# Performance work log

Measured on AMD Instinct MI355X. Metric: run time of the kernel, lower is better.

The kernel has to match this reference:

```python
import jax, jax.numpy as jnp
import numpy as np

N_NODES = 100000
N_EDGES = 3200000
IN_CH, HID, OUT_CH = 11, 64, 1


def setup_inputs() -> dict:
    key = jax.random.key(0)
    ks = jax.random.split(key, 10)
    x = jax.random.normal(ks[0], (N_NODES, IN_CH), dtype=jnp.float32)
    edge_index = jax.random.randint(ks[1], (2, N_EDGES), 0, N_NODES, dtype=jnp.int64)
    s = lambda k, shape, fan_in: jax.random.normal(k, shape, jnp.float32) * (1.0 / np.sqrt(fan_in))
    return {
        "x": x,
        "edge_index": edge_index,
        # conv1: lin_l acts on aggregated neighbors (has bias), lin_r on root (no bias)
        "Wl1": s(ks[2], (HID, IN_CH), IN_CH), "bl1": jnp.zeros((HID,), jnp.float32),
        "Wr1": s(ks[3], (HID, IN_CH), IN_CH),
        "Wl2": s(ks[4], (HID, HID), HID), "bl2": jnp.zeros((HID,), jnp.float32),
        "Wr2": s(ks[5], (HID, HID), HID),
        "Wlin": s(ks[6], (OUT_CH, HID), HID), "blin": jnp.zeros((OUT_CH,), jnp.float32),
    }


def _sage_conv(x, src, dst, Wl, bl, Wr):
    # mean aggregation of source features onto destination nodes
    msg = x[src]                                            # [E, d] gather
    agg = jax.ops.segment_sum(msg, dst, num_segments=N_NODES)          # [N, d]
    cnt = jax.ops.segment_sum(jnp.ones_like(dst, jnp.float32), dst, num_segments=N_NODES)
    mean = agg / jnp.maximum(cnt, 1.0)[:, None]             # isolated nodes -> 0
    return mean @ Wl.T + bl + x @ Wr.T


def reference(x, edge_index, Wl1, bl1, Wr1, Wl2, bl2, Wr2, Wlin, blin):
    src, dst = edge_index[0], edge_index[1]
    h = jax.nn.relu(_sage_conv(x, src, dst, Wl1, bl1, Wr1))
    h = jax.nn.relu(_sage_conv(h, src, dst, Wl2, bl2, Wr2))
    return h @ Wlin.T + blin
```

## Files before the change

### kernel.cpp

```cpp
#include <hip/hip_runtime.h>
#include <hip/hip_fp16.h>

#define IN_CH 11
#define HID 64
#define PAD 64
#define OVCAP 16384
#define NBLK 512
#define BSH 10

typedef _Float16 half8_t __attribute__((ext_vector_type(8)));
typedef float f32x4_t __attribute__((ext_vector_type(4)));

__global__ void k_prep(const float* __restrict__ x, const float* __restrict__ Wl2,
                       const float* __restrict__ Wr2, unsigned* __restrict__ xphu,
                       __half* __restrict__ wl2h, __half* __restrict__ wr2h,
                       int* __restrict__ ovcnt, int N) {
    int i = blockIdx.x * blockDim.x + threadIdx.x;
    if (i == 0) *ovcnt = 0;
    if (i < HID * HID) {
        wl2h[i] = __float2half_rn(Wl2[i]);
        wr2h[i] = __float2half_rn(Wr2[i]);
    }
    if (i < (N + 1) * 8) {
        int n = i >> 3, j = (i & 7) * 2;
        float a = 0.f, b = 0.f;
        if (n < N) {
            if (j < IN_CH) a = x[n * IN_CH + j];
            if (j + 1 < IN_CH) b = x[n * IN_CH + j + 1];
        }
        unsigned lo = (unsigned)__half_as_ushort(__float2half_rn(a));
        unsigned hi = (unsigned)__half_as_ushort(__float2half_rn(b));
        xphu[i] = lo | (hi << 16);
    }
}


__global__ __launch_bounds__(256) void k_hist(const int* __restrict__ dst,
        int* __restrict__ hist, int E, int csz, int nbkt) {
    __shared__ int h[128];
    int tid = threadIdx.x, blk = blockIdx.x;
    if (tid < 128) h[tid] = 0;
    __syncthreads();
    int c0 = blk * csz, c1 = min(c0 + csz, E);
    for (int e = c0 + tid; e < c1; e += 256)
        atomicAdd(&h[dst[e] >> BSH], 1);
    __syncthreads();
    if (tid < nbkt) hist[tid * NBLK + blk] = h[tid];
}

__global__ __launch_bounds__(512) void k_scanA(int* __restrict__ hist,
        int* __restrict__ btot) {
    __shared__ int wsum[8];
    int b = blockIdx.x, tid = threadIdx.x;
    int lane = tid & 63, wv = tid >> 6;
    int v = hist[b * NBLK + tid];
    int inc = v;
    #pragma unroll
    for (int off = 1; off < 64; off <<= 1) {
        int t = __shfl_up(inc, off);
        if (lane >= off) inc += t;
    }
    if (lane == 63) wsum[wv] = inc;
    __syncthreads();
    int base = 0;
    #pragma unroll
    for (int w = 0; w < 8; w++) base += (w < wv) ? wsum[w] : 0;
    hist[b * NBLK + tid] = base + inc - v;
    if (tid == NBLK - 1) btot[b] = base + inc;
}

__global__ __launch_bounds__(128) void k_scanB(const int* __restrict__ btot,
        int* __restrict__ bstart, int nbkt) {
    __shared__ int wsum[2];
    int tid = threadIdx.x;
    int lane = tid & 63, wv = tid >> 6;
    int v = (tid < nbkt) ? btot[tid] : 0;
    int inc = v;
    #pragma unroll
    for (int off = 1; off < 64; off <<= 1) {
        int t = __shfl_up(inc, off);
        if (lane >= off) inc += t;
    }
    if (lane == 63) wsum[wv] = inc;
    __syncthreads();
    int base = (wv == 1) ? wsum[0] : 0;
    if (tid < nbkt) bstart[tid] = base + inc - v;
}

__global__ __launch_bounds__(256) void k_scatter(const int* __restrict__ src,
        const int* __restrict__ dst, const int* __restrict__ hist,
        const int* __restrict__ bstart,
        unsigned* __restrict__ ebuf, int E, int csz, int nbkt) {
    __shared__ int cur[128];
    int tid = threadIdx.x, blk = blockIdx.x;
    if (tid < nbkt) cur[tid] = hist[tid * NBLK + blk] + bstart[tid];
    __syncthreads();
    int c0 = blk * csz, c1 = min(c0 + csz, E);
    for (int e = c0 + tid; e < c1; e += 256) {
        int d = dst[e], s = src[e];
        int slot = atomicAdd(&cur[d >> BSH], 1);
        ebuf[slot] = ((unsigned)(d & 1023) << 17) | (unsigned)s;
    }
}

__global__ __launch_bounds__(1024) void k_bbuild(const unsigned* __restrict__ ebuf,
        const int* __restrict__ bstart, const int* __restrict__ btot,
        int* __restrict__ cnt, int* __restrict__ col64,
        int* __restrict__ ovcnt, int* __restrict__ ov, int N) {
    __shared__ int lc[1024];
    int tid = threadIdx.x, b = blockIdx.x;
    int lo = b << BSH;
    lc[tid] = 0;
    __syncthreads();
    int cs = bstart[b], cc = btot[b];
    for (int i = tid; i < cc; i += 1024) {
        unsigned v = ebuf[cs + i];
        int dl = (int)(v >> 17), s = (int)(v & 0x1FFFFu);
        int r = atomicAdd(&lc[dl], 1);
        if (r < PAD) {
            col64[(size_t)(lo + dl) * PAD + r] = s;
        } else {
            int q = atomicAdd(ovcnt, 1);
            if (q < OVCAP) { ov[2 * q] = lo + dl; ov[2 * q + 1] = s; }
        }
    }
    __syncthreads();
    int n = lo + tid;
    if (n < N) {
        int d = lc[tid];
        cnt[n] = d;
        if (d > PAD) d = PAD;
        int* row = col64 + (size_t)n * PAD;
        for (int r = d; r < PAD; r++) row[r] = N;
    }
}

__global__ void k_agg1(const unsigned* __restrict__ xphu,
                       const int* __restrict__ col64,
                       float* __restrict__ agg1, int N) {
    int lane = threadIdx.x & 63;
    int n = blockIdx.x * 4 + (threadIdx.x >> 6);
    if (n >= N) return;
    int c8 = lane & 7, sub = lane >> 3;
    const int* cb = col64 + n * PAD;
    int s[8];
    #pragma unroll
    for (int jj = 0; jj < 8; jj++) s[jj] = cb[sub + 8 * jj];
    unsigned v[8];
    #pragma unroll
    for (int jj = 0; jj < 8; jj++) v[jj] = xphu[s[jj] * 8 + c8];
    __half2 a2 = __floats2half2_rn(0.f, 0.f);
    #pragma unroll
    for (int jj = 0; jj < 8; jj++) a2 = __hadd2(a2, *(__half2*)&v[jj]);
    float2 f = __half22float2(a2);
    #pragma unroll
    for (int off = 8; off <= 32; off <<= 1) {
        f.x += __shfl_xor(f.x, off);
        f.y += __shfl_xor(f.y, off);
    }
    if (lane < 8) ((float2*)agg1)[n * 8 + lane] = f;
}

__global__ void k_ov1(const int* __restrict__ ovcnt, const int* __restrict__ ov,
                      const float* __restrict__ x, float* __restrict__ agg1) {
    int c = *ovcnt; if (c > OVCAP) c = OVCAP;
    for (int i = blockIdx.x * blockDim.x + threadIdx.x; i < c;
         i += gridDim.x * blockDim.x) {
        int d = ov[2 * i], s = ov[2 * i + 1];
        for (int ch = 0; ch < IN_CH; ch++)
            atomicAdd(&agg1[d * 16 + ch], x[s * IN_CH + ch]);
    }
}

__global__ void k_dense1(const float* __restrict__ x, const float* __restrict__ agg1,
                         const int* __restrict__ cnt, const float* __restrict__ Wl,
                         const float* __restrict__ bl, const float* __restrict__ Wr,
                         unsigned* __restrict__ h1h, int N) {
    int lane = threadIdx.x & 63;
    int n = blockIdx.x * 4 + (threadIdx.x >> 6);
    if (n > N) return;
    if (n == N) {
        if (lane < 32) h1h[n * 32 + lane] = 0u;
        return;
    }
    int deg = cnt[n];
    float inv = deg > 0 ? 1.f / (float)deg : 0.f;
    float mv = (lane < 16) ? agg1[n * 16 + lane] * inv : 0.f;
    float xv = (lane < IN_CH) ? x[n * IN_CH + lane] : 0.f;
    float h = bl[lane];
    #pragma unroll
    for (int c = 0; c < IN_CH; c++)
        h += Wl[lane * IN_CH + c] * __shfl(mv, c) + Wr[lane * IN_CH + c] * __shfl(xv, c);
    h = fmaxf(h, 0.f);
    unsigned my = (unsigned)__half_as_ushort(__float2half_rn(h));
    unsigned nx = __shfl_down(my, 1);
    if ((lane & 1) == 0) h1h[n * 32 + (lane >> 1)] = my | (nx << 16);
}

__global__ void k_agg2(const uint4* __restrict__ h1h4, const int* __restrict__ col64,
                       float* __restrict__ agg2, int N) {
    int lane = threadIdx.x & 63;
    int n = blockIdx.x * 4 + (threadIdx.x >> 6);
    if (n >= N) return;
    int c8 = lane & 7, sub = lane >> 3;
    const int* cb = col64 + n * PAD;
    int s[8];
    #pragma unroll
    for (int jj = 0; jj < 8; jj++) s[jj] = cb[sub + 8 * jj];
    uint4 v[8];
    #pragma unroll
    for (int jj = 0; jj < 8; jj++) v[jj] = h1h4[s[jj] * 8 + c8];
    __half2 a2[4];
    #pragma unroll
    for (int t = 0; t < 4; t++) a2[t] = __floats2half2_rn(0.f, 0.f);
    #pragma unroll
    for (int jj = 0; jj < 8; jj++) {
        a2[0] = __hadd2(a2[0], *(__half2*)&v[jj].x);
        a2[1] = __hadd2(a2[1], *(__half2*)&v[jj].y);
        a2[2] = __hadd2(a2[2], *(__half2*)&v[jj].z);
        a2[3] = __hadd2(a2[3], *(__half2*)&v[jj].w);
    }
    float acc[8];
    #pragma unroll
    for (int t = 0; t < 4; t++) {
        float2 f = __half22float2(a2[t]);
        acc[2 * t] = f.x; acc[2 * t + 1] = f.y;
    }
    #pragma unroll
    for (int off = 8; off <= 32; off <<= 1) {
        #pragma unroll
        for (int t = 0; t < 8; t++) acc[t] += __shfl_xor(acc[t], off);
    }
    float val = acc[0];
    #pragma unroll
    for (int t = 1; t < 8; t++) if (sub == t) val = acc[t];
    agg2[n * 64 + 8 * c8 + sub] = val;
}

__global__ void k_ov2(const int* __restrict__ ovcnt, const int* __restrict__ ov,
                      const unsigned* __restrict__ h1h, float* __restrict__ agg2) {
    int c = *ovcnt; if (c > OVCAP) c = OVCAP;
    const __half* h1 = (const __half*)h1h;
    for (int i = blockIdx.x * blockDim.x + threadIdx.x; i < c;
         i += gridDim.x * blockDim.x) {
        int d = ov[2 * i], s = ov[2 * i + 1];
        for (int ch = 0; ch < HID; ch++)
            atomicAdd(&agg2[d * 64 + ch], __half2float(h1[s * 64 + ch]));
    }
}

__global__ __launch_bounds__(256) void k_dense2(
    const float4* __restrict__ agg2_4, const int* __restrict__ cnt,
    const uint4* __restrict__ h1h_u4,
    const __half* __restrict__ wl2h, const __half* __restrict__ wr2h,
    const float* __restrict__ bl, const float* __restrict__ Wlin,
    const float* __restrict__ blin, float* __restrict__ out, int N) {
    union U { uint4 u; half8_t h; };
    int lane = threadIdx.x & 63;
    int wave = blockIdx.x * 4 + (threadIdx.x >> 6);
    int nwaves = gridDim.x * 4;
    int r16 = lane & 15, quad = lane >> 4;
    const uint4* wlu = (const uint4*)wl2h;
    const uint4* wru = (const uint4*)wr2h;
    half8_t bfr[4][4];
    #pragma unroll
    for (int tt = 0; tt < 4; tt++) {
        int o = tt * 16 + r16;
        U t0, t1, t2, t3;
        t0.u = wlu[o * 8 + quad];
        t1.u = wlu[o * 8 + 4 + quad];
        t2.u = wru[o * 8 + quad];
        t3.u = wru[o * 8 + 4 + quad];
        bfr[tt][0] = t0.h; bfr[tt][1] = t1.h; bfr[tt][2] = t2.h; bfr[tt][3] = t3.h;
    }
    float bl_c[4], wl_c[4];
    #pragma unroll
    for (int tt = 0; tt < 4; tt++) {
        bl_c[tt] = bl[tt * 16 + r16];
        wl_c[tt] = Wlin[tt * 16 + r16];
    }
    float b0 = blin[0];
    int ntiles = (N + 15) >> 4;
    for (int t = wave; t < ntiles; t += nwaves) {
        int nb = t * 16;
        int n = nb + r16; if (n >= N) n = N - 1;
        int deg = cnt[n];
        float inv = deg > 0 ? 1.f / (float)deg : 0.f;
        float4 m0 = agg2_4[n * 16 + quad * 2];
        float4 m1 = agg2_4[n * 16 + quad * 2 + 1];
        float4 m2 = agg2_4[n * 16 + 8 + quad * 2];
        float4 m3 = agg2_4[n * 16 + 8 + quad * 2 + 1];
        half8_t a0h, a1h;
        a0h[0] = (_Float16)(m0.x * inv); a0h[1] = (_Float16)(m0.y * inv);
        a0h[2] = (_Float16)(m0.z * inv); a0h[3] = (_Float16)(m0.w * inv);
        a0h[4] = (_Float16)(m1.x * inv); a0h[5] = (_Float16)(m1.y * inv);
        a0h[6] = (_Float16)(m1.z * inv); a0h[7] = (_Float16)(m1.w * inv);
        a1h[0] = (_Float16)(m2.x * inv); a1h[1] = (_Float16)(m2.y * inv);
        a1h[2] = (_Float16)(m2.z * inv); a1h[3] = (_Float16)(m2.w * inv);
        a1h[4] = (_Float16)(m3.x * inv); a1h[5] = (_Float16)(m3.y * inv);
        a1h[6] = (_Float16)(m3.z * inv); a1h[7] = (_Float16)(m3.w * inv);
        U a2, a3;
        a2.u = h1h_u4[n * 8 + quad];
        a3.u = h1h_u4[n * 8 + 4 + quad];
        float p0 = 0.f, p1 = 0.f, p2 = 0.f, p3 = 0.f;
        #pragma unroll
        for (int tt = 0; tt < 4; tt++) {
            f32x4_t c = {0.f, 0.f, 0.f, 0.f};
            c = __builtin_amdgcn_mfma_f32_16x16x32_f16(a0h, bfr[tt][0], c, 0, 0, 0);
            c = __builtin_amdgcn_mfma_f32_16x16x32_f16(a1h, bfr[tt][1], c, 0, 0, 0);
            c = __builtin_amdgcn_mfma_f32_16x16x32_f16(a2.h, bfr[tt][2], c, 0, 0, 0);
            c = __builtin_amdgcn_mfma_f32_16x16x32_f16(a3.h, bfr[tt][3], c, 0, 0, 0);
            p0 += fmaxf(c[0] + bl_c[tt], 0.f) * wl_c[tt];
            p1 += fmaxf(c[1] + bl_c[tt], 0.f) * wl_c[tt];
            p2 += fmaxf(c[2] + bl_c[tt], 0.f) * wl_c[tt];
            p3 += fmaxf(c[3] + bl_c[tt], 0.f) * wl_c[tt];
        }
        #pragma unroll
        for (int off = 1; off <= 8; off <<= 1) {
            p0 += __shfl_xor(p0, off); p1 += __shfl_xor(p1, off);
            p2 += __shfl_xor(p2, off); p3 += __shfl_xor(p3, off);
        }
        if (r16 == 0) {
            int nn = nb + quad * 4;
            if (nn + 3 < N) {
                ((float4*)out)[nn >> 2] = make_float4(p0 + b0, p1 + b0, p2 + b0, p3 + b0);
            } else {
                if (nn + 0 < N) out[nn + 0] = p0 + b0;
                if (nn + 1 < N) out[nn + 1] = p1 + b0;
                if (nn + 2 < N) out[nn + 2] = p2 + b0;
                if (nn + 3 < N) out[nn + 3] = p3 + b0;
            }
        }
    }
}


extern "C" void kernel_launch(void* const* d_in, const int* in_sizes, int n_in,
                              void* d_out, int out_size, void* d_ws, size_t ws_size,
                              hipStream_t stream) {
    const float* x    = (const float*)d_in[0];
    const int*   ei   = (const int*)d_in[1];
    const float* Wl1  = (const float*)d_in[2];
    const float* bl1  = (const float*)d_in[3];
    const float* Wr1  = (const float*)d_in[4];
    const float* Wl2  = (const float*)d_in[5];
    const float* bl2  = (const float*)d_in[6];
    const float* Wr2  = (const float*)d_in[7];
    const float* Wlin = (const float*)d_in[8];
    const float* blin = (const float*)d_in[9];
    float* out = (float*)d_out;

    int N = in_sizes[0] / IN_CH;
    int E = in_sizes[1] / 2;
    const int* srcp = ei;
    const int* dstp = ei + E;

    int* ws       = (int*)d_ws;
    int* cnt      = ws;
    int* ovcnt    = ws + N;
    int* col64    = ws + 100032;
    int* hist     = ws + 100032;
    unsigned* xph = (unsigned*)(ws + 6500032);
    unsigned* ebuf = (unsigned*)(ws + 7300064);
    float* agg1   = (float*)(ws + 7300064);
    float* agg2   = (float*)(ws + 6500032);
    unsigned* h1h = (unsigned*)(ws + 12900096);
    int* ov       = ws + 16100128;
    __half* wl2h  = (__half*)(ws + 16132896);
    __half* wr2h  = (__half*)(ws + 16134944);
    int* btot     = ws + 16136992;
    int* bstart   = ws + 16138016;

    int nbkt = (N + 1023) >> BSH;
    int csz  = (E + NBLK - 1) / NBLK;

    k_prep   <<<((N + 1) * 8 + 255) / 256, 256, 0, stream>>>(x, Wl2, Wr2, xph,
                                                             wl2h, wr2h, ovcnt, N);
    k_hist   <<<NBLK, 256, 0, stream>>>(dstp, hist, E, csz, nbkt);
    k_scanA  <<<nbkt, NBLK, 0, stream>>>(hist, btot);
    k_scanB  <<<1, 128, 0, stream>>>(btot, bstart, nbkt);
    k_scatter<<<NBLK, 256, 0, stream>>>(srcp, dstp, hist, bstart, ebuf, E, csz, nbkt);
    k_bbuild <<<nbkt, 1024, 0, stream>>>(ebuf, bstart, btot, cnt, col64,
                                         ovcnt, ov, N);

    k_agg1   <<<(N + 3) / 4, 256, 0, stream>>>(xph, col64, agg1, N);
    k_ov1    <<<8, 256, 0, stream>>>(ovcnt, ov, x, agg1);
    k_dense1 <<<(N + 4) / 4, 256, 0, stream>>>(x, agg1, cnt, Wl1, bl1, Wr1, h1h, N);

    k_agg2   <<<(N + 3) / 4, 256, 0, stream>>>((const uint4*)h1h, col64, agg2, N);
    k_ov2    <<<8, 256, 0, stream>>>(ovcnt, ov, h1h, agg2);

    k_dense2 <<<512, 256, 0, stream>>>((const float4*)agg2, cnt, (const uint4*)h1h,
                                       wl2h, wr2h, bl2, Wlin, blin, out, N);
}
```

Measured before the change: 288.4 us.

## Fuse prep/hist and scans, compute layer-1 aggregation in bucket build, skip empty agg2 half

Merges the prep and histogram kernels into one launch, folds the bucket-start scan into the scatter and bucket-build kernels, and removes the separate layer-1 aggregation and overflow kernels by accumulating neighbor features into shared memory with atomics during the bucket build. The layer-2 gather now skips the second half of the padded neighbor list when degree is at most 32. This cuts launches and a full pass over col64 for layer 1. The cost is a 68KB shared array per 1024-thread block, which limits occupancy, plus heavy LDS atomic contention. Layer-1 aggregation now sums in fp32 rather than fp16.

```diff
diff --git a/kernel.cpp b/kernel.cpp
--- a/kernel.cpp
+++ b/kernel.cpp
@@ -11,41 +11,42 @@
 typedef _Float16 half8_t __attribute__((ext_vector_type(8)));
 typedef float f32x4_t __attribute__((ext_vector_type(4)));
 
-__global__ void k_prep(const float* __restrict__ x, const float* __restrict__ Wl2,
-                       const float* __restrict__ Wr2, unsigned* __restrict__ xphu,
-                       __half* __restrict__ wl2h, __half* __restrict__ wr2h,
-                       int* __restrict__ ovcnt, int N) {
-    int i = blockIdx.x * blockDim.x + threadIdx.x;
-    if (i == 0) *ovcnt = 0;
-    if (i < HID * HID) {
-        wl2h[i] = __float2half_rn(Wl2[i]);
-        wr2h[i] = __float2half_rn(Wr2[i]);
-    }
-    if (i < (N + 1) * 8) {
-        int n = i >> 3, j = (i & 7) * 2;
-        float a = 0.f, b = 0.f;
-        if (n < N) {
-            if (j < IN_CH) a = x[n * IN_CH + j];
-            if (j + 1 < IN_CH) b = x[n * IN_CH + j + 1];
-        }
-        unsigned lo = (unsigned)__half_as_ushort(__float2half_rn(a));
-        unsigned hi = (unsigned)__half_as_ushort(__float2half_rn(b));
-        xphu[i] = lo | (hi << 16);
-    }
-}
-
-
-__global__ __launch_bounds__(256) void k_hist(const int* __restrict__ dst,
-        int* __restrict__ hist, int E, int csz, int nbkt) {
+__global__ __launch_bounds__(256) void k_prephist(
+        const float* __restrict__ x, const float* __restrict__ Wl2,
+        const float* __restrict__ Wr2, const int* __restrict__ dst,
+        unsigned* __restrict__ xphu, __half* __restrict__ wl2h,
+        __half* __restrict__ wr2h, int* __restrict__ hist,
+        int* __restrict__ ovcnt, int E, int csz, int nbkt, int N) {
     __shared__ int h[128];
-    int tid = threadIdx.x, blk = blockIdx.x;
-    if (tid < 128) h[tid] = 0;
-    __syncthreads();
-    int c0 = blk * csz, c1 = min(c0 + csz, E);
-    for (int e = c0 + tid; e < c1; e += 256)
-        atomicAdd(&h[dst[e] >> BSH], 1);
-    __syncthreads();
-    if (tid < nbkt) hist[tid * NBLK + blk] = h[tid];
+    int tid = threadIdx.x;
+    if (blockIdx.x < NBLK) {
+        int blk = blockIdx.x;
+        if (tid < 128) h[tid] = 0;
+        __syncthreads();
+        int c0 = blk * csz, c1 = min(c0 + csz, E);
+        for (int e = c0 + tid; e < c1; e += 256)
+            atomicAdd(&h[dst[e] >> BSH], 1);
+        __syncthreads();
+        if (tid < nbkt) hist[tid * NBLK + blk] = h[tid];
+    } else {
+        int i = (blockIdx.x - NBLK) * 256 + tid;
+        if (i == 0) *ovcnt = 0;
+        if (i < HID * HID) {
+            wl2h[i] = __float2half_rn(Wl2[i]);
+            wr2h[i] = __float2half_rn(Wr2[i]);
+        }
+        if (i < (N + 1) * 8) {
+            int n = i >> 3, j = (i & 7) * 2;
+            float a = 0.f, b = 0.f;
+            if (n < N) {
+                if (j < IN_CH) a = x[n * IN_CH + j];
+                if (j + 1 < IN_CH) b = x[n * IN_CH + j + 1];
+            }
+            unsigned lo = (unsigned)__half_as_ushort(__float2half_rn(a));
+            unsigned hi = (unsigned)__half_as_ushort(__float2half_rn(b));
+            xphu[i] = lo | (hi << 16);
+        }
+    }
 }
 
 __global__ __launch_bounds__(512) void k_scanA(int* __restrict__ hist,
@@ -69,31 +70,31 @@
     if (tid == NBLK - 1) btot[b] = base + inc;
 }
 
-__global__ __launch_bounds__(128) void k_scanB(const int* __restrict__ btot,
-        int* __restrict__ bstart, int nbkt) {
-    __shared__ int wsum[2];
-    int tid = threadIdx.x;
-    int lane = tid & 63, wv = tid >> 6;
-    int v = (tid < nbkt) ? btot[tid] : 0;
-    int inc = v;
-    #pragma unroll
-    for (int off = 1; off < 64; off <<= 1) {
-        int t = __shfl_up(inc, off);
-        if (lane >= off) inc += t;
-    }
-    if (lane == 63) wsum[wv] = inc;
-    __syncthreads();
-    int base = (wv == 1) ? wsum[0] : 0;
-    if (tid < nbkt) bstart[tid] = base + inc - v;
-}
-
 __global__ __launch_bounds__(256) void k_scatter(const int* __restrict__ src,
         const int* __restrict__ dst, const int* __restrict__ hist,
-        const int* __restrict__ bstart,
+        const int* __restrict__ btot,
         unsigned* __restrict__ ebuf, int E, int csz, int nbkt) {
     __shared__ int cur[128];
+    __shared__ int wtmp;
     int tid = threadIdx.x, blk = blockIdx.x;
-    if (tid < nbkt) cur[tid] = hist[tid * NBLK + blk] + bstart[tid];
+    int v = 0, inc = 0;
+    if (tid < 128) {
+        int lane = tid & 63;
+        v = (tid < nbkt) ? btot[tid] : 0;
+        inc = v;
+        #pragma unroll
+        for (int off = 1; off < 64; off <<= 1) {
+            int t = __shfl_up(inc, off);
+            if (lane >= off) inc += t;
+        }
+        if (tid == 63) wtmp = inc;
+    }
+    __syncthreads();
+    if (tid < 128) {
+        int base = (tid >= 64) ? wtmp : 0;
+        int bs = base + inc - v;
+        cur[tid] = ((tid < nbkt) ? hist[tid * NBLK + blk] : 0) + bs;
+    }
     __syncthreads();
     int c0 = blk * csz, c1 = min(c0 + csz, E);
     for (int e = c0 + tid; e < c1; e += 256) {
@@ -104,15 +105,27 @@
 }
 
 __global__ __launch_bounds__(1024) void k_bbuild(const unsigned* __restrict__ ebuf,
-        const int* __restrict__ bstart, const int* __restrict__ btot,
-        int* __restrict__ cnt, int* __restrict__ col64,
+        const int* __restrict__ btot, const unsigned* __restrict__ xphu,
+        int* __restrict__ cnt, int* __restrict__ col64, float* __restrict__ agg1,
         int* __restrict__ ovcnt, int* __restrict__ ov, int N) {
+    __shared__ float ash[1024 * 17];
     __shared__ int lc[1024];
+    __shared__ int sbase;
     int tid = threadIdx.x, b = blockIdx.x;
     int lo = b << BSH;
     lc[tid] = 0;
+    #pragma unroll
+    for (int j = 0; j < 17; j++) ash[tid + j * 1024] = 0.f;
+    if (tid < 64) {
+        int s = 0;
+        for (int t = tid; t < b; t += 64) s += btot[t];
+        #pragma unroll
+        for (int off = 32; off >= 1; off >>= 1) s += __shfl_xor(s, off);
+        if (tid == 0) sbase = s;
+    }
     __syncthreads();
-    int cs = bstart[b], cc = btot[b];
+    int cs = sbase, cc = btot[b];
+    const uint4* xq = (const uint4*)xphu;
     for (int i = tid; i < cc; i += 1024) {
         unsigned v = ebuf[cs + i];
         int dl = (int)(v >> 17), s = (int)(v & 0x1FFFFu);
@@ -123,52 +136,30 @@
             int q = atomicAdd(ovcnt, 1);
             if (q < OVCAP) { ov[2 * q] = lo + dl; ov[2 * q + 1] = s; }
         }
+        uint4 u0 = xq[s * 2], u1 = xq[s * 2 + 1];
+        float* arow = &ash[dl * 17];
+        float2 f;
+        f = __half22float2(*(__half2*)&u0.x); atomicAdd(&arow[0], f.x); atomicAdd(&arow[1], f.y);
+        f = __half22float2(*(__half2*)&u0.y); atomicAdd(&arow[2], f.x); atomicAdd(&arow[3], f.y);
+        f = __half22float2(*(__half2*)&u0.z); atomicAdd(&arow[4], f.x); atomicAdd(&arow[5], f.y);
+        f = __half22float2(*(__half2*)&u0.w); atomicAdd(&arow[6], f.x); atomicAdd(&arow[7], f.y);
+        f = __half22float2(*(__half2*)&u1.x); atomicAdd(&arow[8], f.x); atomicAdd(&arow[9], f.y);
+        f = __half22float2(*(__half2*)&u1.y); atomicAdd(&arow[10], f.x);
     }
     __syncthreads();
     int n = lo + tid;
     if (n < N) {
         int d = lc[tid];
         cnt[n] = d;
-        if (d > PAD) d = PAD;
+        int dc = min(d, PAD);
         int* row = col64 + (size_t)n * PAD;
-        for (int r = d; r < PAD; r++) row[r] = N;
-    }
-}
-
-__global__ void k_agg1(const unsigned* __restrict__ xphu,
-                       const int* __restrict__ col64,
-                       float* __restrict__ agg1, int N) {
-    int lane = threadIdx.x & 63;
-    int n = blockIdx.x * 4 + (threadIdx.x >> 6);
-    if (n >= N) return;
-    int c8 = lane & 7, sub = lane >> 3;
-    const int* cb = col64 + n * PAD;
-    int s[8];
-    #pragma unroll
-    for (int jj = 0; jj < 8; jj++) s[jj] = cb[sub + 8 * jj];
-    unsigned v[8];
-    #pragma unroll
-    for (int jj = 0; jj < 8; jj++) v[jj] = xphu[s[jj] * 8 + c8];
-    __half2 a2 = __floats2half2_rn(0.f, 0.f);
-    #pragma unroll
-    for (int jj = 0; jj < 8; jj++) a2 = __hadd2(a2, *(__half2*)&v[jj]);
-    float2 f = __half22float2(a2);
-    #pragma unroll
-    for (int off = 8; off <= 32; off <<= 1) {
-        f.x += __shfl_xor(f.x, off);
-        f.y += __shfl_xor(f.y, off);
-    }
-    if (lane < 8) ((float2*)agg1)[n * 8 + lane] = f;
-}
-
-__global__ void k_ov1(const int* __restrict__ ovcnt, const int* __restrict__ ov,
-                      const float* __restrict__ x, float* __restrict__ agg1) {
-    int c = *ovcnt; if (c > OVCAP) c = OVCAP;
-    for (int i = blockIdx.x * blockDim.x + threadIdx.x; i < c;
-         i += gridDim.x * blockDim.x) {
-        int d = ov[2 * i], s = ov[2 * i + 1];
-        for (int ch = 0; ch < IN_CH; ch++)
-            atomicAdd(&agg1[d * 16 + ch], x[s * IN_CH + ch]);
+        for (int r = dc; r < PAD; r++) row[r] = N;
+    }
+    #pragma unroll
+    for (int j = 0; j < 16; j++) {
+        int idx = tid + j * 1024;
+        int nl = idx >> 4, ch = idx & 15;
+        if (lo + nl < N) agg1[(size_t)(lo + nl) * 16 + ch] = ash[nl * 17 + ch];
     }
 }
 
@@ -198,27 +189,45 @@
 }
 
 __global__ void k_agg2(const uint4* __restrict__ h1h4, const int* __restrict__ col64,
-                       float* __restrict__ agg2, int N) {
+                       const int* __restrict__ cnt, float* __restrict__ agg2, int N) {
     int lane = threadIdx.x & 63;
     int n = blockIdx.x * 4 + (threadIdx.x >> 6);
     if (n >= N) return;
     int c8 = lane & 7, sub = lane >> 3;
     const int* cb = col64 + n * PAD;
-    int s[8];
-    #pragma unroll
-    for (int jj = 0; jj < 8; jj++) s[jj] = cb[sub + 8 * jj];
-    uint4 v[8];
-    #pragma unroll
-    for (int jj = 0; jj < 8; jj++) v[jj] = h1h4[s[jj] * 8 + c8];
+    int deg = cnt[n];
     __half2 a2[4];
     #pragma unroll
     for (int t = 0; t < 4; t++) a2[t] = __floats2half2_rn(0.f, 0.f);
-    #pragma unroll
-    for (int jj = 0; jj < 8; jj++) {
-        a2[0] = __hadd2(a2[0], *(__half2*)&v[jj].x);
-        a2[1] = __hadd2(a2[1], *(__half2*)&v[jj].y);
-        a2[2] = __hadd2(a2[2], *(__half2*)&v[jj].z);
-        a2[3] = __hadd2(a2[3], *(__half2*)&v[jj].w);
+    {
+        int s[4];
+        #pragma unroll
+        for (int jj = 0; jj < 4; jj++) s[jj] = cb[sub + 8 * jj];
+        uint4 v[4];
+        #pragma unroll
+        for (int jj = 0; jj < 4; jj++) v[jj] = h1h4[s[jj] * 8 + c8];
+        #pragma unroll
+        for (int jj = 0; jj < 4; jj++) {
+            a2[0] = __hadd2(a2[0], *(__half2*)&v[jj].x);
+            a2[1] = __hadd2(a2[1], *(__half2*)&v[jj].y);
+            a2[2] = __hadd2(a2[2], *(__half2*)&v[jj].z);
+            a2[3] = __hadd2(a2[3], *(__half2*)&v[jj].w);
+        }
+    }
+    if (deg > 32) {
+        int s[4];
+        #pragma unroll
+        for (int jj = 0; jj < 4; jj++) s[jj] = cb[sub + 8 * (4 + jj)];
+        uint4 v[4];
+        #pragma unroll
+        for (int jj = 0; jj < 4; jj++) v[jj] = h1h4[s[jj] * 8 + c8];
+        #pragma unroll
+        for (int jj = 0; jj < 4; jj++) {
+            a2[0] = __hadd2(a2[0], *(__half2*)&v[jj].x);
+            a2[1] = __hadd2(a2[1], *(__half2*)&v[jj].y);
+            a2[2] = __hadd2(a2[2], *(__half2*)&v[jj].z);
+            a2[3] = __hadd2(a2[3], *(__half2*)&v[jj].w);
+        }
     }
     float acc[8];
     #pragma unroll
@@ -355,39 +364,37 @@
     const int* srcp = ei;
     const int* dstp = ei + E;
 
-    int* ws       = (int*)d_ws;
-    int* cnt      = ws;
-    int* ovcnt    = ws + N;
-    int* col64    = ws + 100032;
-    int* hist     = ws + 100032;
-    unsigned* xph = (unsigned*)(ws + 6500032);
+    int* ws        = (int*)d_ws;
+    int* cnt       = ws;
+    int* ovcnt     = ws + N;
+    int* col64     = ws + 100032;
+    int* hist      = ws + 100032;
+    unsigned* xph  = (unsigned*)(ws + 6500032);
     unsigned* ebuf = (unsigned*)(ws + 7300064);
-    float* agg1   = (float*)(ws + 7300064);
-    float* agg2   = (float*)(ws + 6500032);
-    unsigned* h1h = (unsigned*)(ws + 12900096);
-    int* ov       = ws + 16100128;
-    __half* wl2h  = (__half*)(ws + 16132896);
-    __half* wr2h  = (__half*)(ws + 16134944);
-    int* btot     = ws + 16136992;
-    int* bstart   = ws + 16138016;
+    float* agg1    = (float*)(ws + 10500064);
+    float* agg2    = (float*)(ws + 6500032);
+    unsigned* h1h  = (unsigned*)(ws + 12900096);
+    int* ov        = ws + 16100128;
+    __half* wl2h   = (__half*)(ws + 16132896);
+    __half* wr2h   = (__half*)(ws + 16134944);
+    int* btot      = ws + 16136992;
 
     int nbkt = (N + 1023) >> BSH;
     int csz  = (E + NBLK - 1) / NBLK;
-
-    k_prep   <<<((N + 1) * 8 + 255) / 256, 256, 0, stream>>>(x, Wl2, Wr2, xph,
-                                                             wl2h, wr2h, ovcnt, N);
-    k_hist   <<<NBLK, 256, 0, stream>>>(dstp, hist, E, csz, nbkt);
+    int prep_blocks = ((N + 1) * 8 + 255) / 256;
+
+    k_prephist<<<NBLK + prep_blocks, 256, 0, stream>>>(x, Wl2, Wr2, dstp, xph,
+                                                       wl2h, wr2h, hist, ovcnt,
+                                                       E, csz, nbkt, N);
     k_scanA  <<<nbkt, NBLK, 0, stream>>>(hist, btot);
-    k_scanB  <<<1, 128, 0, stream>>>(btot, bstart, nbkt);
-    k_scatter<<<NBLK, 256, 0, stream>>>(srcp, dstp, hist, bstart, ebuf, E, csz, nbkt);
-    k_bbuild <<<nbkt, 1024, 0, stream>>>(ebuf, bstart, btot, cnt, col64,
+    k_scatter<<<NBLK, 256, 0, stream>>>(srcp, dstp, hist, btot, ebuf, E, csz, nbkt);
+    k_bbuild <<<nbkt, 1024, 0, stream>>>(ebuf, btot, xph, cnt, col64, agg1,
                                          ovcnt, ov, N);
 
-    k_agg1   <<<(N + 3) / 4, 256, 0, stream>>>(xph, col64, agg1, N);
-    k_ov1    <<<8, 256, 0, stream>>>(ovcnt, ov, x, agg1);
     k_dense1 <<<(N + 4) / 4, 256, 0, stream>>>(x, agg1, cnt, Wl1, bl1, Wr1, h1h, N);
 
-    k_agg2   <<<(N + 3) / 4, 256, 0, stream>>>((const uint4*)h1h, col64, agg2, N);
+    k_agg2   <<<(N + 3) / 4, 256, 0, stream>>>((const uint4*)h1h, col64, cnt,
+                                               agg2, N);
     k_ov2    <<<8, 256, 0, stream>>>(ovcnt, ov, h1h, agg2);
 
     k_dense2 <<<512, 256, 0, stream>>>((const float4*)agg2, cnt, (const uint4*)h1h,
```

Result: slower. 692.7 us (+140.2%).
